# Performance work log

Measured on AMD Instinct MI355X. Metric: run time of the kernel, lower is better.

Reference implementation:

```python
import math
import jax, jax.numpy as jnp
import numpy as np

RMS_EPS = 1.1920929e-07  # torch.finfo(float32).eps used by F.rms_norm default

def _rms_norm(x):
    return x * jax.lax.rsqrt(jnp.mean(jnp.square(x), axis=-1, keepdims=True) + RMS_EPS)

def _rope(x, cos, sin):
    # x: [B,T,H,D]; cos/sin: [T, D//2]
    d = x.shape[-1] // 2
    x1, x2 = x[..., :d], x[..., d:]
    c = cos[None, :, None, :]
    s = sin[None, :, None, :]
    return jnp.concatenate([x1 * c + x2 * s, -x1 * s + x2 * c], axis=-1).astype(x.dtype)

def setup_inputs():
    key = jax.random.key(0)
    ks = jax.random.split(key, 8)
    B, T, C, H, D = 2, 2048, 2048, 16, 128
    x = jax.random.normal(ks[0], (B, T, C), dtype=jnp.float32)
    # real RoPE tables for [T, D//2]
    half = D // 2
    inv_freq = 1.0 / (10000.0 ** (np.arange(half, dtype=np.float32) / half))
    ang = np.outer(np.arange(T, dtype=np.float32), inv_freq)
    cos = jnp.asarray(np.cos(ang), dtype=jnp.float32)
    sin = jnp.asarray(np.sin(ang), dtype=jnp.float32)
    s = 0.02
    Wq = jax.random.normal(ks[1], (C, H * D), dtype=jnp.float32) * s
    Wk = jax.random.normal(ks[2], (C, H * D), dtype=jnp.float32) * s
    Wv = jax.random.normal(ks[3], (C, H * D), dtype=jnp.float32) * s
    Wo = jax.random.normal(ks[4], (C, C), dtype=jnp.float32) * s
    fgate_w = jax.random.normal(ks[5], (C, H), dtype=jnp.float32) * s
    fgate_b = jnp.zeros((H,), dtype=jnp.float32)
    weight_lambda = jax.random.normal(ks[6], (C, H), dtype=jnp.float32) * s
    return dict(x=x, cos=cos, sin=sin, Wq=Wq, Wk=Wk, Wv=Wv, Wo=Wo,
                fgate_w=fgate_w, fgate_b=fgate_b, weight_lambda=weight_lambda,
                window_size=1024)

def reference(x, cos, sin, Wq, Wk, Wv, Wo, fgate_w, fgate_b, weight_lambda, window_size):
    B, T, C = x.shape
    H = fgate_w.shape[1]
    D = Wq.shape[1] // H
    sm_scale = 1.0 / math.sqrt(D)
    # QKV projections (bias=False)
    q = (x @ Wq).reshape(B, T, H, D)
    k = (x @ Wk).reshape(B, T, H, D)
    v = (x @ Wv).reshape(B, T, H, D)
    # RoPE then parameter-free RMSNorm on q,k
    q = _rms_norm(_rope(q, cos, sin))
    k = _rms_norm(_rope(k, cos, sin))
    # [B,H,T,D]
    q = q.transpose(0, 2, 1, 3)
    k = k.transpose(0, 2, 1, 3)
    v = v.transpose(0, 2, 1, 3)
    # forgetting gate: log f_t per (B,H,T)
    lam = jax.nn.elu((x @ weight_lambda).astype(jnp.float32)) + 1.0          # [B,T,H]
    logit = (x @ fgate_w + fgate_b) * lam                                    # [B,T,H]
    log_fgate = (jax.nn.log_sigmoid(logit) / (lam + 0.001)).transpose(0, 2, 1)  # [B,H,T]
    cumF = jnp.cumsum(log_fgate, axis=-1)                                    # [B,H,T]
    # forgetting flash attention, dense reference: bias_ij = cumF_i - cumF_j
    scores = jnp.einsum('bhqd,bhkd->bhqk', q.astype(jnp.float32), k.astype(jnp.float32)) * sm_scale
    scores = scores + cumF[..., :, None] - cumF[..., None, :]
    i = jnp.arange(T)[:, None]
    j = jnp.arange(T)[None, :]
    allowed = (j <= i) & (i - j < window_size)  # causal + sliding window
    scores = jnp.where(allowed, scores, -jnp.inf)
    attn = jax.nn.softmax(scores, axis=-1)
    y = jnp.einsum('bhqk,bhkd->bhqd', attn, v.astype(jnp.float32)).astype(x.dtype)
    y = y.transpose(0, 2, 1, 3).reshape(B, T, C)
    return y @ Wo
```

## Files before the change

### kernel.cpp

```cpp
#include <hip/hip_runtime.h>
#include <hip/hip_bf16.h>
#include <stdint.h>

#define T_SEQ 2048
#define CDIM  2048
#define NHEAD 16
#define DHEAD 128
#define BT    4096
#define BHT   32
#define NQKV  6144
#define LOG2E 1.4426950408889634f

typedef __bf16 bf16x8_t __attribute__((ext_vector_type(8)));
typedef float  f32x4_t  __attribute__((ext_vector_type(4)));
typedef unsigned short u16x8_t __attribute__((ext_vector_type(8)));
typedef unsigned short u16x4_t __attribute__((ext_vector_type(4)));
typedef unsigned int   u32x4_t __attribute__((ext_vector_type(4)));

__device__ __forceinline__ unsigned short f2bf(float f){
  unsigned int u = __float_as_uint(f);
  u += 0x7fffu + ((u >> 16) & 1u);
  return (unsigned short)(u >> 16);
}
__device__ __forceinline__ float bf2f(unsigned short h){
  return __uint_as_float(((unsigned int)h) << 16);
}
__device__ __forceinline__ unsigned ldsaddr(const void* p){
  return (unsigned)(size_t)(const __attribute__((address_space(3))) void*)p;
}
__device__ __forceinline__ u16x4_t tr16(unsigned a){
  u16x4_t r;
  asm volatile("ds_read_b64_tr_b16 %0, %1" : "=v"(r) : "v"(a));
  return r;
}

__global__ __launch_bounds__(256) void transpose_cast(const float* __restrict__ W,
                                                      unsigned short* __restrict__ Wt){
  __shared__ float tile[32][33];
  int n0 = blockIdx.x*32, k0 = blockIdx.y*32;
  int tx = threadIdx.x, ty = threadIdx.y;
  #pragma unroll
  for (int i=0;i<32;i+=8)
    tile[ty+i][tx] = W[(size_t)(k0+ty+i)*CDIM + n0 + tx];
  __syncthreads();
  #pragma unroll
  for (int i=0;i<32;i+=8)
    Wt[(size_t)(n0+ty+i)*CDIM + k0 + tx] = f2bf(tile[tx][ty+i]);
}

__global__ __launch_bounds__(256) void build_wgt(const float* __restrict__ fgw,
                                                 const float* __restrict__ wlam,
                                                 float* __restrict__ WgT){
  int idx = blockIdx.x*256 + threadIdx.x;
  int c = idx >> 11, k = idx & 2047;
  const float* W = (c < 16) ? fgw : wlam;
  WgT[idx] = W[k*16 + (c & 15)];
}


#define V3_SYNC() do{ __builtin_amdgcn_sched_barrier(0); \
  __builtin_amdgcn_s_barrier(); \
  asm volatile("s_waitcnt lgkmcnt(0)" ::: "memory"); \
  __builtin_amdgcn_sched_barrier(0); }while(0)

#define V3_TAIL() do{ asm volatile("s_waitcnt vmcnt(3)" ::: "memory"); \
  __builtin_amdgcn_sched_barrier(0); \
  __builtin_amdgcn_s_barrier(); }while(0)

#define V3_MFMA() do{ __builtin_amdgcn_s_setprio(1); \
  _Pragma("unroll") for (int mi=0;mi<4;mi++) \
  _Pragma("unroll") for (int ni=0;ni<4;ni++) \
    acc[mi][ni] = __builtin_amdgcn_mfma_f32_16x16x32_bf16(af[mi], bfr[ni], acc[mi][ni],0,0,0); \
  __builtin_amdgcn_s_setprio(0); }while(0)

#define V3_PHASE(BUF, TIDX) do{ \
  readA(BUF); readB(BUF); \
  { int ts_ = (TIDX)+2; if (ts_ > ntm1) ts_ = ntm1; stage(((BUF)+2)%3, ts_); } \
  V3_SYNC(); V3_MFMA(); V3_TAIL(); }while(0)

template<int MODE>
__global__ __launch_bounds__(512, 2) void gemm_v3(const unsigned short* __restrict__ A,
                                                  const unsigned short* __restrict__ Bt,
                                                  void* __restrict__ Cout,
                                                  int M, int N, int K){
  extern __shared__ unsigned short lds[];
  const int nx = N >> 8;
  const int Mt = M >> 7;
  const int bid = blockIdx.x;
  const int c8 = bid & 7, w = bid >> 3;
  const int mh = Mt >> 1;
  const int mt = (c8 & 1)*mh + (w % mh);
  const int ntc = (c8 >> 1)*(nx >> 2) + (w / mh);
  const int m0 = mt << 7, n0 = ntc << 8;
  const int tid = threadIdx.x, lane = tid & 63, wv = tid >> 6;
  const int wm = wv >> 2, wn = wv & 3;
  const int g = lane >> 4, qi = lane & 15;
  const int ntm1 = (K >> 5) - 1;

  f32x4_t acc[4][4] = {};
  bf16x8_t af[4], bfr[4];

  int goffA, goffB[2];
  { int s = tid; int row = s >> 2; int lg = (s & 3) ^ ((row >> 1) & 3);
    goffA = row*K + lg*8; }
  #pragma unroll
  for (int j=0;j<2;j++){
    int s = j*512 + tid;
    int row = s >> 2;
    int lg = (s & 3) ^ ((row >> 1) & 3);
    goffB[j] = row*K + lg*8;
  }

  auto stage = [&](int buf, int kt){
    const unsigned short* srcA = A + (size_t)m0*K + kt*32;
    const unsigned short* srcB = Bt + (size_t)n0*K + kt*32;
    unsigned short* base = lds + buf*12288;
    __builtin_amdgcn_global_load_lds(
        (const __attribute__((address_space(1))) void*)(srcA + goffA),
        (__attribute__((address_space(3))) void*)(base + tid*8), 16, 0, 0);
    #pragma unroll
    for (int j=0;j<2;j++)
      __builtin_amdgcn_global_load_lds(
        (const __attribute__((address_space(1))) void*)(srcB + goffB[j]),
        (__attribute__((address_space(3))) void*)(base + 4096 + (j*512 + tid)*8), 16, 0, 0);
  };
  auto readA = [&](int buf){
    const unsigned short* base = lds + buf*12288;
    #pragma unroll
    for (int mi=0;mi<4;mi++){
      int row = wm*64 + mi*16 + qi;
      int gs = g ^ ((row >> 1) & 3);
      af[mi] = *reinterpret_cast<const bf16x8_t*>(base + (row*4 + gs)*8);
    }
  };
  auto readB = [&](int buf){
    const unsigned short* base = lds + buf*12288 + 4096;
    #pragma unroll
    for (int ni=0;ni<4;ni++){
      int row = wn*64 + ni*16 + qi;
      int gs = g ^ ((row >> 1) & 3);
      bfr[ni] = *reinterpret_cast<const bf16x8_t*>(base + (row*4 + gs)*8);
    }
  };

  stage(0,0); stage(1,1);
  asm volatile("s_waitcnt vmcnt(3)" ::: "memory");
  __builtin_amdgcn_sched_barrier(0);
  __builtin_amdgcn_s_barrier();

  for (int it=0; it<21; ++it){
    const int t3 = it*3;
    V3_PHASE(0, t3+0);
    V3_PHASE(1, t3+1);
    V3_PHASE(2, t3+2);
  }
  V3_PHASE(0, 63);
  asm volatile("s_waitcnt vmcnt(0)" ::: "memory");

  #pragma unroll
  for (int mi=0;mi<4;mi++){
    #pragma unroll
    for (int ni=0;ni<4;ni++){
      #pragma unroll
      for (int r=0;r<4;r++){
        int mm = m0 + wm*64 + mi*16 + 4*g + r;
        int nn = n0 + wn*64 + ni*16 + qi;
        float v = acc[mi][ni][r];
        if (MODE == 2){
          ((float*)Cout)[(size_t)mm*N + nn] = v;
        } else {
          int bb2 = mm >> 11, t = mm & (T_SEQ-1);
          int which = nn >> 11;
          int hh = (nn >> 7) & 15, d = nn & (DHEAD-1);
          ((unsigned short*)Cout)[(size_t)which*8388608 +
              (((size_t)bb2*NHEAD + hh)*T_SEQ + t)*DHEAD + d] = f2bf(v);
        }
      }
    }
  }
}


#define W_SYNC() V3_SYNC()
#define W_TAIL() do{ asm volatile("s_waitcnt vmcnt(2)" ::: "memory"); \
  __builtin_amdgcn_sched_barrier(0); \
  __builtin_amdgcn_s_barrier(); }while(0)

#define W_MFMA() do{ __builtin_amdgcn_s_setprio(1); \
  _Pragma("unroll") for (int mi=0;mi<4;mi++) \
  _Pragma("unroll") for (int ni=0;ni<2;ni++) \
    acc[mi][ni] = __builtin_amdgcn_mfma_f32_16x16x32_bf16(af[mi], bfr[ni], acc[mi][ni],0,0,0); \
  __builtin_amdgcn_s_setprio(0); }while(0)

#define W_PHASE(BUF, TIDX) do{ \
  readA(BUF); readB(BUF); \
  { int ts_ = (TIDX)+2; if (ts_ > ntm1) ts_ = ntm1; stage(((BUF)+2)%3, ts_); } \
  W_SYNC(); W_MFMA(); W_TAIL(); }while(0)

__global__ __launch_bounds__(512, 2) void gemm_w(const unsigned short* __restrict__ A,
                                                 const unsigned short* __restrict__ Bt,
                                                 float* __restrict__ Cout,
                                                 int M, int N, int K){
  extern __shared__ unsigned short lds[];
  const int nx = N >> 7;
  const int Mt = M >> 7;
  const int bid = blockIdx.x;
  const int c8 = bid & 7, w = bid >> 3;
  const int mh = Mt >> 1;
  const int mt = (c8 & 1)*mh + (w % mh);
  const int ntc = (c8 >> 1)*(nx >> 2) + (w / mh);
  const int m0 = mt << 7, n0 = ntc << 7;
  const int tid = threadIdx.x, lane = tid & 63, wv = tid >> 6;
  const int wm = wv >> 2, wn = wv & 3;
  const int g = lane >> 4, qi = lane & 15;
  const int ntm1 = (K >> 5) - 1;

  f32x4_t acc[4][2] = {};
  bf16x8_t af[4], bfr[2];

  int goff;
  { int s = tid; int row = s >> 2; int lg = (s & 3) ^ ((row >> 1) & 3);
    goff = row*K + lg*8; }

  auto stage = [&](int buf, int kt){
    const unsigned short* srcA = A + (size_t)m0*K + kt*32;
    const unsigned short* srcB = Bt + (size_t)n0*K + kt*32;
    unsigned short* base = lds + buf*8192;
    __builtin_amdgcn_global_load_lds(
        (const __attribute__((address_space(1))) void*)(srcA + goff),
        (__attribute__((address_space(3))) void*)(base + tid*8), 16, 0, 0);
    __builtin_amdgcn_global_load_lds(
        (const __attribute__((address_space(1))) void*)(srcB + goff),
        (__attribute__((address_space(3))) void*)(base + 4096 + tid*8), 16, 0, 0);
  };
  auto readA = [&](int buf){
    const unsigned short* base = lds + buf*8192;
    #pragma unroll
    for (int mi=0;mi<4;mi++){
      int row = wm*64 + mi*16 + qi;
      int gs = g ^ ((row >> 1) & 3);
      af[mi] = *reinterpret_cast<const bf16x8_t*>(base + (row*4 + gs)*8);
    }
  };
  auto readB = [&](int buf){
    const unsigned short* base = lds + buf*8192 + 4096;
    #pragma unroll
    for (int ni=0;ni<2;ni++){
      int row = wn*32 + ni*16 + qi;
      int gs = g ^ ((row >> 1) & 3);
      bfr[ni] = *reinterpret_cast<const bf16x8_t*>(base + (row*4 + gs)*8);
    }
  };

  stage(0,0); stage(1,1);
  asm volatile("s_waitcnt vmcnt(2)" ::: "memory");
  __builtin_amdgcn_sched_barrier(0);
  __builtin_amdgcn_s_barrier();

  for (int it=0; it<21; ++it){
    const int t3 = it*3;
    W_PHASE(0, t3+0);
    W_PHASE(1, t3+1);
    W_PHASE(2, t3+2);
  }
  W_PHASE(0, 63);
  asm volatile("s_waitcnt vmcnt(0)" ::: "memory");

  #pragma unroll
  for (int mi=0;mi<4;mi++){
    #pragma unroll
    for (int ni=0;ni<2;ni++){
      #pragma unroll
      for (int r=0;r<4;r++){
        int mm = m0 + wm*64 + mi*16 + 4*g + r;
        int nn = n0 + wn*32 + ni*16 + qi;
        Cout[(size_t)mm*N + nn] = acc[mi][ni][r];
      }
    }
  }
}

#define GROWS 4
__global__ __launch_bounds__(256) void gates_kernel(const float* __restrict__ x,
    const float* __restrict__ WgT, const float* __restrict__ fgb,
    float* __restrict__ lfg, unsigned short* __restrict__ xb){
  __shared__ float xs[GROWS*2048];
  __shared__ float part[GROWS*32*8];
  const int r0 = blockIdx.x*GROWS;
  const int tid = threadIdx.x;
  const float* xp = x + (size_t)r0*CDIM;
  #pragma unroll
  for (int i=0;i<GROWS*2048/(256*4); i++){
    int e = (i*256+tid)*4;
    *(float4*)(xs+e) = *(const float4*)(xp+e);
  }
  __syncthreads();
  #pragma unroll
  for (int i=0;i<GROWS*2048/(256*8); i++){
    int e = (i*256+tid)*8;
    u16x8_t ob;
    #pragma unroll
    for (int j=0;j<8;j++) ob[j] = f2bf(xs[e+j]);
    *reinterpret_cast<u16x8_t*>(xb + (size_t)r0*CDIM + e) = ob;
  }
  const int c = tid & 31, kseg = tid >> 5;
  const float* wp = WgT + c*2048 + kseg*256;
  const float* xq = xs + kseg*256;
  f32x4_t acc[GROWS] = {};
  for (int kk=0; kk<64; kk++){
    f32x4_t wv = *(const f32x4_t*)(wp + kk*4);
    #pragma unroll
    for (int r=0;r<GROWS;r++){
      f32x4_t xv = *(const f32x4_t*)(xq + r*2048 + kk*4);
      acc[r] += xv*wv;
    }
  }
  #pragma unroll
  for (int r=0;r<GROWS;r++)
    part[(r*32 + c)*8 + kseg] = acc[r][0]+acc[r][1]+acc[r][2]+acc[r][3];
  __syncthreads();
  if (tid < GROWS*32){
    const int r = tid >> 5, c2 = tid & 31;
    const float* pp = part + (r*32+c2)*8;
    float s = pp[0]+pp[1]+pp[2]+pp[3]+pp[4]+pp[5]+pp[6]+pp[7];
    float other = __shfl_xor(s, 16, 64);
    if (c2 < 16){
      float df = s, dl = other;
      float lam = (dl > 0.f) ? (dl + 1.f) : __expf(dl);
      float logit = (df + fgb[c2]) * lam;
      float ls = fminf(logit, 0.f) - log1pf(__expf(-fabsf(logit)));
      float lf = ls / (lam + 0.001f);
      int row = r0 + r;
      int b = row >> 11, t = row & (T_SEQ-1);
      lfg[((size_t)b*NHEAD + c2)*T_SEQ + t] = lf;
    }
  }
}

__global__ __launch_bounds__(256) void cumsum_kernel(const float* __restrict__ lfg,
                                                     float* __restrict__ cumF){
  __shared__ float sums[256];
  const int bh = blockIdx.x;
  const float* in = lfg + (size_t)bh*T_SEQ;
  float* out = cumF + (size_t)bh*T_SEQ;
  const int tid = threadIdx.x;
  float4 a = *(const float4*)(in + tid*8);
  float4 b = *(const float4*)(in + tid*8 + 4);
  float v[8] = {a.x,a.y,a.z,a.w,b.x,b.y,b.z,b.w};
  float run = 0.f;
  #pragma unroll
  for (int e=0;e<8;e++) run += v[e];
  sums[tid] = run;
  __syncthreads();
  for (int off=1; off<256; off<<=1){
    float y = (tid >= off) ? sums[tid-off] : 0.f;
    __syncthreads();
    sums[tid] += y;
    __syncthreads();
  }
  float acc = sums[tid] - run;
  float o[8];
  #pragma unroll
  for (int e=0;e<8;e++){ acc += v[e]; o[e] = acc*LOG2E; }
  *(float4*)(out + tid*8)     = make_float4(o[0],o[1],o[2],o[3]);
  *(float4*)(out + tid*8 + 4) = make_float4(o[4],o[5],o[6],o[7]);
}

__global__ __launch_bounds__(256) void rope_rms(unsigned short* __restrict__ QK,
    const float* __restrict__ cosT, const float* __restrict__ sinT){
  const int tid = threadIdx.x, lane = tid & 63, wv = tid >> 6;
  const int idx2 = blockIdx.x*4 + wv;
  const int which = idx2 >> 16;
  const int row = idx2 & 65535;
  const int t = row & (T_SEQ-1);
  unsigned short* xp = QK + (size_t)which*8388608 + (size_t)row*DHEAD;
  float x1 = bf2f(xp[lane]);
  float x2 = bf2f(xp[lane+64]);
  float c = cosT[t*64 + lane];
  float s = sinT[t*64 + lane];
  float o1 = x1*c + x2*s;
  float o2 = x2*c - x1*s;
  float ss = o1*o1 + o2*o2;
  #pragma unroll
  for (int off=1; off<64; off<<=1) ss += __shfl_xor(ss, off, 64);
  float scale = rsqrtf(ss*(1.f/128.f) + 1.1920929e-07f);
  xp[lane]    = f2bf(o1*scale);
  xp[lane+64] = f2bf(o2*scale);
}

__global__ __launch_bounds__(256, 2) void attn_kernel(const unsigned short* __restrict__ Qh,
    const unsigned short* __restrict__ Kh, const unsigned short* __restrict__ Vh,
    const float* __restrict__ cumF, unsigned short* __restrict__ Y,
    const int* __restrict__ winp){
  __shared__ unsigned short smem[32768];
  const int dlin = blockIdx.y*16 + blockIdx.x;
  const int c8 = dlin & 7, klin = dlin >> 3;
  const int bh = c8 + 8*(klin >> 4);
  const int q0b = (klin & 15)*128;
  const int b = bh >> 4, h = bh & 15;
  const int tid = threadIdx.x, lane = tid & 63, wv = tid >> 6;
  const int g = lane >> 4, qi = lane & 15;
  const int win = *winp;
  const unsigned short* Qp = Qh + (size_t)bh*T_SEQ*DHEAD;
  const unsigned short* Kp = Kh + (size_t)bh*T_SEQ*DHEAD;
  const unsigned short* Vp = Vh + (size_t)bh*T_SEQ*DHEAD;
  const float* cF = cumF + (size_t)bh*T_SEQ;
  const int q0w = q0b + wv*32;
  bf16x8_t qf[2][4];
  float cFq[2];
  #pragma unroll
  for (int qb=0;qb<2;qb++){
    cFq[qb] = cF[q0w + qb*16 + qi];
    #pragma unroll
    for (int dt=0;dt<4;dt++)
      qf[qb][dt] = *reinterpret_cast<const bf16x8_t*>(Qp + (size_t)(q0w + qb*16 + qi)*DHEAD + dt*32 + g*8);
  }
  f32x4_t ot[2][8] = {};
  float mrun[2] = {-1e30f, -1e30f}, lrun[2] = {0.f, 0.f};
  const float sm2 = 0.08838834764831845f * LOG2E;
  int kbeg = q0b - win + 1; if (kbeg < 0) kbeg = 0; kbeg &= ~63;
  const int nt = (q0b + 128 - kbeg) >> 6;

  auto stage = [&](int bi, int k0s){
    unsigned short* Kd = smem + bi*8192;
    unsigned short* Vd = smem + 16384 + bi*8192;
    #pragma unroll
    for (int jj=0;jj<4;jj++){
      int t = (wv*4+jj)*64 + lane;
      int r = t>>4, cc = t&15;
      __builtin_amdgcn_global_load_lds(
        (const __attribute__((address_space(1))) void*)(Kp + (size_t)(k0s+r)*DHEAD + ((cc ^ (r&7))*8)),
        (__attribute__((address_space(3))) void*)(Kd + t*8), 16, 0, 0);
      int dd = t>>7, kq = (t>>3)&15, rr = (t>>1)&3, hb = t&1;
      __builtin_amdgcn_global_load_lds(
        (const __attribute__((address_space(1))) void*)(Vp + (size_t)(k0s + kq*4 + rr)*DHEAD + dd*16 + hb*8),
        (__attribute__((address_space(3))) void*)(Vd + t*8), 16, 0, 0);
    }
  };

  stage(0, kbeg);
  for (int it=0; it<nt; ++it){
    const int k0 = kbeg + it*64;
    const int cur = it & 1;
    __syncthreads();
    if (it+1 < nt) stage(cur^1, k0+64);
    if (k0 <= q0w+31 && (k0 + 63) >= (q0w - win + 1)){
      const unsigned short* Kc = smem + cur*8192;
      f32x4_t s[2][4] = {};
      __builtin_amdgcn_s_setprio(1);
      #pragma unroll
      for (int dt=0;dt<4;dt++){
        bf16x8_t kf[4];
        #pragma unroll
        for (int kb=0;kb<4;kb++){
          int row = kb*16 + qi;
          kf[kb] = *reinterpret_cast<const bf16x8_t*>(Kc + row*128 + (((dt*4+g) ^ (row&7))*8));
        }
        #pragma unroll
        for (int kb=0;kb<4;kb++){
          s[0][kb] = __builtin_amdgcn_mfma_f32_16x16x32_bf16(kf[kb], qf[0][dt], s[0][kb], 0,0,0);
          s[1][kb] = __builtin_amdgcn_mfma_f32_16x16x32_bf16(kf[kb], qf[1][dt], s[1][kb], 0,0,0);
        }
      }
      __builtin_amdgcn_s_setprio(0);
      float4 cb[4];
      #pragma unroll
      for (int kb=0;kb<4;kb++) cb[kb] = *(const float4*)(cF + k0 + kb*16 + 4*g);
      const bool interior = (k0 + 63 <= q0w) && (k0 >= q0w + 32 - win);
      u32x4_t pbw[2][2];
      #pragma unroll
      for (int qb=0;qb<2;qb++){
        const int qg = q0w + qb*16 + qi;
        float p[16], tmax = -INFINITY;
        if (interior){
          #pragma unroll
          for (int kb=0;kb<4;kb++){
            #pragma unroll
            for (int r=0;r<4;r++){
              float sv = fmaf(s[qb][kb][r], sm2, cFq[qb] - ((const float*)&cb[kb])[r]);
              p[kb*4+r] = sv;
              tmax = fmaxf(tmax, sv);
            }
          }
        } else {
          #pragma unroll
          for (int kb=0;kb<4;kb++){
            #pragma unroll
            for (int r=0;r<4;r++){
              int key = k0 + kb*16 + 4*g + r;
              float sv = fmaf(s[qb][kb][r], sm2, cFq[qb] - ((const float*)&cb[kb])[r]);
              bool ok = (key <= qg) && (qg - key < win);
              p[kb*4+r] = ok ? sv : -INFINITY;
              tmax = fmaxf(tmax, p[kb*4+r]);
            }
          }
        }
        tmax = fmaxf(tmax, __shfl_xor(tmax, 16, 64));
        tmax = fmaxf(tmax, __shfl_xor(tmax, 32, 64));
        if (__any(tmax > mrun[qb])){
          float mnew = fmaxf(mrun[qb], tmax);
          float alpha = exp2f(mrun[qb] - mnew);
          lrun[qb] *= alpha;
          #pragma unroll
          for (int dt=0;dt<8;dt++) ot[qb][dt] *= alpha;
          mrun[qb] = mnew;
        }
        float tsum = 0.f;
        #pragma unroll
        for (int i2=0;i2<16;i2++){ p[i2] = exp2f(p[i2] - mrun[qb]); tsum += p[i2]; }
        tsum += __shfl_xor(tsum, 16, 64);
        tsum += __shfl_xor(tsum, 32, 64);
        lrun[qb] += tsum;
        #pragma unroll
        for (int cc=0;cc<2;cc++){
          #pragma unroll
          for (int j=0;j<4;j++){
            unsigned wpk;
            asm("v_cvt_pk_bf16_f32 %0, %1, %2" : "=v"(wpk)
                : "v"(p[8*cc+2*j]), "v"(p[8*cc+2*j+1]));
            pbw[qb][cc][j] = wpk;
          }
        }
      }
      unsigned vbase = ldsaddr(smem + 16384 + cur*8192) + lane*8;
      #pragma unroll
      for (int cc=0;cc<2;cc++){
        u16x4_t vlo[8], vhi[8];
        #pragma unroll
        for (int dt=0;dt<8;dt++){
          vlo[dt] = tr16(vbase + (unsigned)((dt*16 + 8*cc)*128));
          vhi[dt] = tr16(vbase + (unsigned)((dt*16 + 8*cc + 4)*128));
        }
        asm volatile("s_waitcnt lgkmcnt(0)");
        __builtin_amdgcn_sched_barrier(0);
        __builtin_amdgcn_s_setprio(1);
        #pragma unroll
        for (int dt=0;dt<8;dt++){
          u16x8_t vv = __builtin_shufflevector(vlo[dt], vhi[dt], 0,1,2,3,4,5,6,7);
          bf16x8_t vf = *reinterpret_cast<bf16x8_t*>(&vv);
          ot[0][dt] = __builtin_amdgcn_mfma_f32_16x16x32_bf16(vf, *reinterpret_cast<bf16x8_t*>(&pbw[0][cc]), ot[0][dt], 0,0,0);
          ot[1][dt] = __builtin_amdgcn_mfma_f32_16x16x32_bf16(vf, *reinterpret_cast<bf16x8_t*>(&pbw[1][cc]), ot[1][dt], 0,0,0);
        }
        __builtin_amdgcn_s_setprio(0);
      }
    }
  }
  __syncthreads();
  float invl[2] = {1.f/lrun[0], 1.f/lrun[1]};
  #pragma unroll
  for (int qb=0;qb<2;qb++){
    int qlocal = wv*32 + qb*16 + qi;
    #pragma unroll
    for (int dt=0;dt<8;dt++){
      int d8 = dt*2 + (g>>1);
      u16x4_t w;
      #pragma unroll
      for (int r=0;r<4;r++) w[r] = f2bf(ot[qb][dt][r]*invl[qb]);
      *reinterpret_cast<u16x4_t*>(smem + qlocal*128 + ((d8 ^ (qlocal&7))*8) + 4*(g&1)) = w;
    }
  }
  __syncthreads();
  #pragma unroll
  for (int i=0;i<8;i++){
    int t = i*256 + tid;
    int row = t>>4, cc = t&15;
    u16x8_t v = *reinterpret_cast<const u16x8_t*>(smem + row*128 + ((cc ^ (row&7))*8));
    *reinterpret_cast<u16x8_t*>(Y + ((size_t)b*T_SEQ + q0b + row)*CDIM + h*DHEAD + cc*8) = v;
  }
}

extern "C" void kernel_launch(void* const* d_in, const int* in_sizes, int n_in,
                              void* d_out, int out_size, void* d_ws, size_t ws_size,
                              hipStream_t stream){
  const float* x    = (const float*)d_in[0];
  const float* cosT = (const float*)d_in[1];
  const float* sinT = (const float*)d_in[2];
  const float* Wq   = (const float*)d_in[3];
  const float* Wk   = (const float*)d_in[4];
  const float* Wv   = (const float*)d_in[5];
  const float* Wo   = (const float*)d_in[6];
  const float* fgw  = (const float*)d_in[7];
  const float* fgb  = (const float*)d_in[8];
  const float* wlam = (const float*)d_in[9];
  const int*   winp = (const int*)d_in[10];

  char* ws = (char*)d_ws;
  unsigned short* xb    = (unsigned short*)(ws + 0);
  unsigned short* WqkvT = (unsigned short*)(ws + 16777216);
  unsigned short* WoT   = (unsigned short*)(ws + 41943040);
  unsigned short* QKVh  = (unsigned short*)(ws + 50331648);
  unsigned short* Qh = QKVh;
  unsigned short* Kh = QKVh + 8388608;
  unsigned short* Vh = QKVh + 16777216;
  unsigned short* Yb  = (unsigned short*)(ws + 100663296);
  float* lfg  = (float*)(ws + 117440512);
  float* cumF = (float*)(ws + 117702656);
  float* WgT  = (float*)(ws + 117964800);

  build_wgt<<<256, 256, 0, stream>>>(fgw, wlam, WgT);
  gates_kernel<<<BT/GROWS, 256, 0, stream>>>(x, WgT, fgb, lfg, xb);
  cumsum_kernel<<<BHT, 256, 0, stream>>>(lfg, cumF);

  dim3 tgrid(64,64), tblk(32,8);
  transpose_cast<<<tgrid, tblk, 0, stream>>>(Wq, WqkvT);
  transpose_cast<<<tgrid, tblk, 0, stream>>>(Wk, WqkvT + 4194304);
  transpose_cast<<<tgrid, tblk, 0, stream>>>(Wv, WqkvT + 8388608);
  transpose_cast<<<tgrid, tblk, 0, stream>>>(Wo, WoT);

  hipFuncSetAttribute(reinterpret_cast<const void*>(&gemm_v3<1>),
      hipFuncAttributeMaxDynamicSharedMemorySize, 73728);
  hipFuncSetAttribute(reinterpret_cast<const void*>(&gemm_w),
      hipFuncAttributeMaxDynamicSharedMemorySize, 49152);

  gemm_v3<1><<<(BT/128)*(NQKV/256), 512, 73728, stream>>>(xb, WqkvT, QKVh, BT, NQKV, CDIM);

  rope_rms<<<2*BHT*T_SEQ/4, 256, 0, stream>>>(QKVh, cosT, sinT);

  attn_kernel<<<dim3(16, BHT), 256, 0, stream>>>(Qh, Kh, Vh, cumF, Yb, winp);

  gemm_w<<<(BT/128)*(CDIM/128), 512, 49152, stream>>>(Yb, WoT, (float*)d_out, BT, CDIM, CDIM);
}
```

Measured before the change: 298.1 us.

## Retile QKV GEMM to 128x192 and use 128x256 tiles for output projection

Adds a 384-thread QKV GEMM kernel with 128x192 tiles. The grid grows from 768 to 1024 blocks, which is meant to balance better across CUs at two blocks per CU; the A/B staging is spread over four load slots per thread, with the fourth issued only by the first 128 threads. The output projection drops the 128x128 gemm_w kernel and reuses gemm_v3 in fp32-store mode with 128x256 tiles, giving one block per CU with more reuse per tile. The risks are the uneven load distribution in the new kernel and lower occupancy in the output GEMM.

```diff
diff --git a/kernel.cpp b/kernel.cpp
--- a/kernel.cpp
+++ b/kernel.cpp
@@ -57,7 +57,6 @@
   WgT[idx] = W[k*16 + (c & 15)];
 }
 
-
 #define V3_SYNC() do{ __builtin_amdgcn_sched_barrier(0); \
   __builtin_amdgcn_s_barrier(); \
   asm volatile("s_waitcnt lgkmcnt(0)" ::: "memory"); \
@@ -77,6 +76,105 @@
   readA(BUF); readB(BUF); \
   { int ts_ = (TIDX)+2; if (ts_ > ntm1) ts_ = ntm1; stage(((BUF)+2)%3, ts_); } \
   V3_SYNC(); V3_MFMA(); V3_TAIL(); }while(0)
+
+__global__ __launch_bounds__(384, 2) void gemm_qkv(const unsigned short* __restrict__ A,
+                                                   const unsigned short* __restrict__ Bt,
+                                                   unsigned short* __restrict__ Cout,
+                                                   int M, int N, int K){
+  extern __shared__ unsigned short lds[];
+  const int nx = N / 192;
+  const int Mt = M >> 7;
+  const int bid = blockIdx.x;
+  const int c8 = bid & 7, w = bid >> 3;
+  const int mh = Mt >> 1;
+  const int mt = (c8 & 1)*mh + (w % mh);
+  const int ntc = (c8 >> 1)*(nx >> 2) + (w / mh);
+  const int m0 = mt << 7, n0 = ntc * 192;
+  const int tid = threadIdx.x, lane = tid & 63, wv = tid >> 6;
+  const int wm = wv / 3, wn = wv % 3;
+  const int g = lane >> 4, qi = lane & 15;
+  const int ntm1 = (K >> 5) - 1;
+
+  f32x4_t acc[4][4] = {};
+  bf16x8_t af[4], bfr[4];
+
+  const unsigned short* baseA = A + (size_t)m0*K;
+  const unsigned short* baseB = Bt + (size_t)n0*K;
+  const unsigned short* gp[4]; int lo[4];
+  #pragma unroll
+  for (int j=0;j<4;j++){
+    int s = j*384 + tid;
+    bool ok = (s < 1280);
+    int si = (s >= 512) ? s - 512 : s;
+    int row = si >> 2;
+    int lg = (si & 3) ^ ((row >> 1) & 3);
+    const unsigned short* bp = (s >= 512) ? baseB : baseA;
+    gp[j] = ok ? (bp + row*K + lg*8) : baseA;
+    lo[j] = ok ? (((s >= 512) ? 4096 : 0) + si*8) : 0;
+  }
+
+  auto stage = [&](int buf, int kt){
+    unsigned short* base = lds + buf*10240;
+    #pragma unroll
+    for (int j=0;j<3;j++)
+      __builtin_amdgcn_global_load_lds(
+        (const __attribute__((address_space(1))) void*)(gp[j] + kt*32),
+        (__attribute__((address_space(3))) void*)(base + lo[j]), 16, 0, 0);
+    if (tid < 128)
+      __builtin_amdgcn_global_load_lds(
+        (const __attribute__((address_space(1))) void*)(gp[3] + kt*32),
+        (__attribute__((address_space(3))) void*)(base + lo[3]), 16, 0, 0);
+  };
+  auto readA = [&](int buf){
+    const unsigned short* base = lds + buf*10240;
+    #pragma unroll
+    for (int mi=0;mi<4;mi++){
+      int row = wm*64 + mi*16 + qi;
+      int gs = g ^ ((row >> 1) & 3);
+      af[mi] = *reinterpret_cast<const bf16x8_t*>(base + (row*4 + gs)*8);
+    }
+  };
+  auto readB = [&](int buf){
+    const unsigned short* base = lds + buf*10240 + 4096;
+    #pragma unroll
+    for (int ni=0;ni<4;ni++){
+      int row = wn*64 + ni*16 + qi;
+      int gs = g ^ ((row >> 1) & 3);
+      bfr[ni] = *reinterpret_cast<const bf16x8_t*>(base + (row*4 + gs)*8);
+    }
+  };
+
+  stage(0,0); stage(1,1);
+  asm volatile("s_waitcnt vmcnt(3)" ::: "memory");
+  __builtin_amdgcn_sched_barrier(0);
+  __builtin_amdgcn_s_barrier();
+
+  for (int it=0; it<21; ++it){
+    const int t3 = it*3;
+    V3_PHASE(0, t3+0);
+    V3_PHASE(1, t3+1);
+    V3_PHASE(2, t3+2);
+  }
+  V3_PHASE(0, 63);
+  asm volatile("s_waitcnt vmcnt(0)" ::: "memory");
+
+  #pragma unroll
+  for (int mi=0;mi<4;mi++){
+    #pragma unroll
+    for (int ni=0;ni<4;ni++){
+      #pragma unroll
+      for (int r=0;r<4;r++){
+        int mm = m0 + wm*64 + mi*16 + 4*g + r;
+        int nn = n0 + wn*64 + ni*16 + qi;
+        int bb2 = mm >> 11, t = mm & (T_SEQ-1);
+        int which = nn >> 11;
+        int hh = (nn >> 7) & 15, d = nn & (DHEAD-1);
+        Cout[(size_t)which*8388608 +
+            (((size_t)bb2*NHEAD + hh)*T_SEQ + t)*DHEAD + d] = f2bf(acc[mi][ni][r]);
+      }
+    }
+  }
+}
 
 template<int MODE>
 __global__ __launch_bounds__(512, 2) void gemm_v3(const unsigned short* __restrict__ A,
@@ -175,106 +273,6 @@
           ((unsigned short*)Cout)[(size_t)which*8388608 +
               (((size_t)bb2*NHEAD + hh)*T_SEQ + t)*DHEAD + d] = f2bf(v);
         }
-      }
-    }
-  }
-}
-
-
-#define W_SYNC() V3_SYNC()
-#define W_TAIL() do{ asm volatile("s_waitcnt vmcnt(2)" ::: "memory"); \
-  __builtin_amdgcn_sched_barrier(0); \
-  __builtin_amdgcn_s_barrier(); }while(0)
-
-#define W_MFMA() do{ __builtin_amdgcn_s_setprio(1); \
-  _Pragma("unroll") for (int mi=0;mi<4;mi++) \
-  _Pragma("unroll") for (int ni=0;ni<2;ni++) \
-    acc[mi][ni] = __builtin_amdgcn_mfma_f32_16x16x32_bf16(af[mi], bfr[ni], acc[mi][ni],0,0,0); \
-  __builtin_amdgcn_s_setprio(0); }while(0)
-
-#define W_PHASE(BUF, TIDX) do{ \
-  readA(BUF); readB(BUF); \
-  { int ts_ = (TIDX)+2; if (ts_ > ntm1) ts_ = ntm1; stage(((BUF)+2)%3, ts_); } \
-  W_SYNC(); W_MFMA(); W_TAIL(); }while(0)
-
-__global__ __launch_bounds__(512, 2) void gemm_w(const unsigned short* __restrict__ A,
-                                                 const unsigned short* __restrict__ Bt,
-                                                 float* __restrict__ Cout,
-                                                 int M, int N, int K){
-  extern __shared__ unsigned short lds[];
-  const int nx = N >> 7;
-  const int Mt = M >> 7;
-  const int bid = blockIdx.x;
-  const int c8 = bid & 7, w = bid >> 3;
-  const int mh = Mt >> 1;
-  const int mt = (c8 & 1)*mh + (w % mh);
-  const int ntc = (c8 >> 1)*(nx >> 2) + (w / mh);
-  const int m0 = mt << 7, n0 = ntc << 7;
-  const int tid = threadIdx.x, lane = tid & 63, wv = tid >> 6;
-  const int wm = wv >> 2, wn = wv & 3;
-  const int g = lane >> 4, qi = lane & 15;
-  const int ntm1 = (K >> 5) - 1;
-
-  f32x4_t acc[4][2] = {};
-  bf16x8_t af[4], bfr[2];
-
-  int goff;
-  { int s = tid; int row = s >> 2; int lg = (s & 3) ^ ((row >> 1) & 3);
-    goff = row*K + lg*8; }
-
-  auto stage = [&](int buf, int kt){
-    const unsigned short* srcA = A + (size_t)m0*K + kt*32;
-    const unsigned short* srcB = Bt + (size_t)n0*K + kt*32;
-    unsigned short* base = lds + buf*8192;
-    __builtin_amdgcn_global_load_lds(
-        (const __attribute__((address_space(1))) void*)(srcA + goff),
-        (__attribute__((address_space(3))) void*)(base + tid*8), 16, 0, 0);
-    __builtin_amdgcn_global_load_lds(
-        (const __attribute__((address_space(1))) void*)(srcB + goff),
-        (__attribute__((address_space(3))) void*)(base + 4096 + tid*8), 16, 0, 0);
-  };
-  auto readA = [&](int buf){
-    const unsigned short* base = lds + buf*8192;
-    #pragma unroll
-    for (int mi=0;mi<4;mi++){
-      int row = wm*64 + mi*16 + qi;
-      int gs = g ^ ((row >> 1) & 3);
-      af[mi] = *reinterpret_cast<const bf16x8_t*>(base + (row*4 + gs)*8);
-    }
-  };
-  auto readB = [&](int buf){
-    const unsigned short* base = lds + buf*8192 + 4096;
-    #pragma unroll
-    for (int ni=0;ni<2;ni++){
-      int row = wn*32 + ni*16 + qi;
-      int gs = g ^ ((row >> 1) & 3);
-      bfr[ni] = *reinterpret_cast<const bf16x8_t*>(base + (row*4 + gs)*8);
-    }
-  };
-
-  stage(0,0); stage(1,1);
-  asm volatile("s_waitcnt vmcnt(2)" ::: "memory");
-  __builtin_amdgcn_sched_barrier(0);
-  __builtin_amdgcn_s_barrier();
-
-  for (int it=0; it<21; ++it){
-    const int t3 = it*3;
-    W_PHASE(0, t3+0);
-    W_PHASE(1, t3+1);
-    W_PHASE(2, t3+2);
-  }
-  W_PHASE(0, 63);
-  asm volatile("s_waitcnt vmcnt(0)" ::: "memory");
-
-  #pragma unroll
-  for (int mi=0;mi<4;mi++){
-    #pragma unroll
-    for (int ni=0;ni<2;ni++){
-      #pragma unroll
-      for (int r=0;r<4;r++){
-        int mm = m0 + wm*64 + mi*16 + 4*g + r;
-        int nn = n0 + wn*32 + ni*16 + qi;
-        Cout[(size_t)mm*N + nn] = acc[mi][ni][r];
       }
     }
   }
@@ -607,16 +605,16 @@
   transpose_cast<<<tgrid, tblk, 0, stream>>>(Wv, WqkvT + 8388608);
   transpose_cast<<<tgrid, tblk, 0, stream>>>(Wo, WoT);
 
-  hipFuncSetAttribute(reinterpret_cast<const void*>(&gemm_v3<1>),
+  hipFuncSetAttribute(reinterpret_cast<const void*>(&gemm_qkv),
+      hipFuncAttributeMaxDynamicSharedMemorySize, 61440);
+  hipFuncSetAttribute(reinterpret_cast<const void*>(&gemm_v3<2>),
       hipFuncAttributeMaxDynamicSharedMemorySize, 73728);
-  hipFuncSetAttribute(reinterpret_cast<const void*>(&gemm_w),
-      hipFuncAttributeMaxDynamicSharedMemorySize, 49152);
-
-  gemm_v3<1><<<(BT/128)*(NQKV/256), 512, 73728, stream>>>(xb, WqkvT, QKVh, BT, NQKV, CDIM);
+
+  gemm_qkv<<<(BT/128)*(NQKV/192), 384, 61440, stream>>>(xb, WqkvT, QKVh, BT, NQKV, CDIM);
 
   rope_rms<<<2*BHT*T_SEQ/4, 256, 0, stream>>>(QKVh, cosT, sinT);
 
   attn_kernel<<<dim3(16, BHT), 256, 0, stream>>>(Qh, Kh, Vh, cumF, Yb, winp);
 
-  gemm_w<<<(BT/128)*(CDIM/128), 512, 49152, stream>>>(Yb, WoT, (float*)d_out, BT, CDIM, CDIM);
-}
+  gemm_v3<2><<<(BT/128)*(CDIM/256), 512, 73728, stream>>>(Yb, WoT, d_out, BT, CDIM, CDIM);
+}
```

Result: slower. 318.2 us (+6.8%).
